# Optimization experiments

Measured on AMD Instinct MI355X. Metric: run time of the kernel, lower is better.

Reference implementation:

```python
import jax, jax.numpy as jnp
import numpy as np

# MORR all-pass ring parameters (MORRConfig_20um defaults: attenuation / self-coupling)
A_MORR = 0.8578
R_MORR = 0.8578
KS = 3       # kernel_size
MB = 8       # miniblock (circulant block size)
BN_EPS = 1e-5


def mrr_roundtrip_phase_to_tr(phi):
    # through-port transmission of an all-pass microring vs roundtrip phase
    c = jnp.cos(phi)
    num = A_MORR * A_MORR - 2.0 * A_MORR * R_MORR * c + R_MORR * R_MORR
    den = 1.0 - 2.0 * A_MORR * R_MORR * c + (A_MORR * R_MORR) ** 2
    return num / den


def setup_inputs() -> dict:
    key = jax.random.key(0)
    k1, k2 = jax.random.split(key, 2)
    B, C, H, W = 64, 64, 32, 32
    outC = 64
    q = (C * KS * KS + MB - 1) // MB   # grid_dim_x = 72
    p = (outC + MB - 1) // MB          # grid_dim_y = 8
    x = jax.random.normal(k1, (B, C, H, W), jnp.float32)
    weight = jax.random.normal(k2, (p, q, MB), jnp.float32) * 0.05  # circulant eigen-vectors per block
    gamma = jnp.ones((outC,), jnp.float32)   # BatchNorm2d weight
    beta = jnp.zeros((outC,), jnp.float32)   # BatchNorm2d bias
    return {"x": x, "weight": weight, "gamma": gamma, "beta": beta}


def reference(x, weight, gamma, beta):
    B, C, H, W = x.shape
    p, q, mb = weight.shape
    outC = gamma.shape[0]
    Ho, Wo = H, W  # stride=1, padding=1, ks=3
    L = Ho * Wo
    # im2col (torch F.unfold ordering: C major, then kh, kw)
    xp = jnp.pad(x, ((0, 0), (0, 0), (1, 1), (1, 1)))
    cols = jnp.stack([xp[:, :, i:i + Ho, j:j + Wo]
                      for i in range(KS) for j in range(KS)], axis=2)  # [B,C,9,Ho,Wo]
    cols = cols.reshape(B, C * KS * KS, L).transpose(0, 2, 1)          # [B,L,C*k*k]
    assert C * KS * KS == q * mb, "patch dim must pad to q*mb"
    s = cols.reshape(B, L, q, mb)
    s = s * s  # optical intensity (power) fed into the MORR
    # block-circulant weight: Wc[p,q,i,j] = weight[p,q,(i-j) mod mb]
    i_idx = jnp.arange(mb)
    idx = (i_idx[:, None] - i_idx[None, :]) % mb
    Wc = weight[:, :, idx]                                             # [p,q,mb,mb]
    # accumulated roundtrip phase per output node
    phase = jnp.einsum('blqj,pqij->blpi', s, Wc)                       # [B,L,p,mb]
    tr = mrr_roundtrip_phase_to_tr(phase)
    out = tr.reshape(B, L, p * mb)[:, :, :outC]                        # truncate to out_channel
    out = out.transpose(0, 2, 1).reshape(B, outC, Ho, Wo)
    # BatchNorm2d (training mode: batch statistics) + Hardtanh(-1, 1)
    mean = out.mean(axis=(0, 2, 3), keepdims=True)
    var = out.var(axis=(0, 2, 3), keepdims=True)
    y = (out - mean) * jax.lax.rsqrt(var + BN_EPS)
    y = y * gamma[None, :, None, None] + beta[None, :, None, None]
    return jnp.clip(y, -1.0, 1.0)
```

## Files before the change

### kernel.cpp

```cpp
#include <hip/hip_runtime.h>


#define A_MORR 0.8578f
#define R_MORR 0.8578f
#define TR_C1 (A_MORR * A_MORR + R_MORR * R_MORR)
#define TR_C2 (-2.0f * A_MORR * R_MORR)
#define TR_C3 (1.0f + (A_MORR * R_MORR) * (A_MORR * R_MORR))
#define BN_EPS 1e-5f

#define NPIX 65536
#define X2_LO 17408
#define SMEM_BYTES 34816
#define NBLK 1024

typedef __attribute__((ext_vector_type(8))) short bf16x8;
typedef __attribute__((ext_vector_type(16))) float f32x16;

__device__ __forceinline__ void bf16split(float s, unsigned short& h, unsigned short& l) {
    union { float f; unsigned u; } cv; cv.f = s;
    unsigned r = (cv.u + 0x7fffu + ((cv.u >> 16) & 1u)) & 0xffff0000u;
    h = (unsigned short)(r >> 16);
    union { unsigned u; float f; } hv; hv.u = r;
    float lo = s - hv.f;
    cv.f = lo;
    unsigned r2 = cv.u + 0x7fffu + ((cv.u >> 16) & 1u);
    l = (unsigned short)(r2 >> 16);
}

__global__ __launch_bounds__(256) void prep_kernel(const float* __restrict__ w,
                                                   char* __restrict__ wfrag) {
    int gtid = blockIdx.x * 256 + threadIdx.x;
    if (gtid < 36864) {
        int j    = gtid & 7;
        int lane = (gtid >> 3) & 63;
        int okm  = gtid >> 9;
        int mt   = okm & 1;
        int ks   = (okm >> 1) & 3;
        int off  = okm >> 3;
        int oc   = mt * 32 + (lane & 31);
        int c    = ks * 16 + (lane >> 5) * 8 + j;
        int kg   = c * 9 + off;
        float val = w[(oc >> 3) * 576 + (kg >> 3) * 8 + ((oc - kg) & 7)];
        unsigned short h, l;
        bf16split(val, h, l);
        ((unsigned short*)(wfrag + okm * 2048))[lane * 8 + j] = h;
        ((unsigned short*)(wfrag + okm * 2048 + 1024))[lane * 8 + j] = l;
    }
}

__global__ __launch_bounds__(256, 4) void conv_kernel(const float* __restrict__ x,
                                                      const char* __restrict__ wfrag,
                                                      float* __restrict__ out,
                                                      float* __restrict__ partials) {
    const int rt  = blockIdx.x;
    const int b   = blockIdx.y;
    const int bid = b * 16 + rt;
    const int tid = threadIdx.x;

    const int lane = tid & 63;
    const int wv   = tid >> 6;
    const int wmt  = wv & 1;
    const int py   = wv >> 1;
    const int col  = lane & 31;
    const int hs   = lane >> 5;

    __shared__ __align__(16) char smem[SMEM_BYTES];

    if (tid < 128) {
        int pr = tid & 1;
        int q  = (tid >> 1) & 7;
        int rc = tid >> 4;
        int r  = rc >> 1;
        int cc = (rc & 1) ? 33 : 0;
        int g  = q ^ (cc & 7);
        *(uint4*)(smem + pr * X2_LO + ((r * 34 + cc) << 7) + (g << 4)) = uint4{0, 0, 0, 0};
    }

    {
        const int co = tid & 31;
        const int qg = tid >> 5;
        const int c  = 1 + co;
        const int gw = (qg ^ (c & 7)) << 4;
        const float* xb = x + (size_t)(b * 64 + qg * 8) * 1024 + co;
#pragma unroll
        for (int r = 0; r < 4; ++r) {
            int gr = rt * 2 - 1 + r;
            float v[8];
#pragma unroll
            for (int j = 0; j < 8; ++j) v[j] = 0.0f;
            if (gr >= 0 && gr < 32) {
#pragma unroll
                for (int j = 0; j < 8; ++j) v[j] = xb[j * 1024 + gr * 32];
            }
            unsigned hp[4], lp[4];
#pragma unroll
            for (int p = 0; p < 4; ++p) {
                unsigned short h0, l0, h1, l1;
                float s0 = v[2 * p] * v[2 * p];
                float s1 = v[2 * p + 1] * v[2 * p + 1];
                bf16split(s0, h0, l0);
                bf16split(s1, h1, l1);
                hp[p] = (unsigned)h0 | ((unsigned)h1 << 16);
                lp[p] = (unsigned)l0 | ((unsigned)l1 << 16);
            }
            char* dst = smem + ((r * 34 + c) << 7) + gw;
            *(uint4*)dst            = uint4{hp[0], hp[1], hp[2], hp[3]};
            *(uint4*)(dst + X2_LO)  = uint4{lp[0], lp[1], lp[2], lp[3]};
        }
    }
    __syncthreads();

    f32x16 acc;
#pragma unroll
    for (int i = 0; i < 16; ++i) acc[i] = 0.f;

    const char* wbase = wfrag + wmt * 2048 + (size_t)lane * 16;

#pragma unroll
    for (int dj = 0; dj < 3; ++dj) {
        const int c2 = col + dj;
        const int c7 = c2 & 7;
#pragma unroll
        for (int kp = 0; kp < 2; ++kp) {
            bf16x8 wh_[2][3], wl_[2][3];
#pragma unroll
            for (int ksi = 0; ksi < 2; ++ksi) {
#pragma unroll
                for (int di = 0; di < 3; ++di) {
                    const char* wp = wbase + (di * 3 + dj) * 16384 + (kp * 2 + ksi) * 4096;
                    wh_[ksi][di] = *(const bf16x8*)wp;
                    wl_[ksi][di] = *(const bf16x8*)(wp + 1024);
                }
            }
#pragma unroll
            for (int ksi = 0; ksi < 2; ++ksi) {
                const int ks = kp * 2 + ksi;
                const int gg = ((ks * 2 + hs) ^ c7) << 4;
                bf16x8 bh[3], bl[3];
#pragma unroll
                for (int di = 0; di < 3; ++di) {
                    const char* sp = smem + (((py + di) * 34 + c2) << 7) + gg;
                    bh[di] = *(const bf16x8*)sp;
                    bl[di] = *(const bf16x8*)(sp + X2_LO);
                }
#pragma unroll
                for (int di = 0; di < 3; ++di) {
                    acc = __builtin_amdgcn_mfma_f32_32x32x16_bf16(wh_[ksi][di], bh[di], acc, 0, 0, 0);
                    acc = __builtin_amdgcn_mfma_f32_32x32x16_bf16(wh_[ksi][di], bl[di], acc, 0, 0, 0);
                    acc = __builtin_amdgcn_mfma_f32_32x32x16_bf16(wl_[ksi][di], bh[di], acc, 0, 0, 0);
                }
            }
        }
    }

    float tv[16];
    {
        const size_t obase = ((size_t)b * 64 + wmt * 32) * 1024 + (rt * 2 + py) * 32 + col;
#pragma unroll
        for (int j = 0; j < 16; ++j) {
            float cp = __cosf(acc[j]);
            float t  = fmaf(TR_C2, cp, TR_C1) / fmaf(TR_C2, cp, TR_C3);
            tv[j] = t;
            int ocl = (j & 3) + 8 * (j >> 2) + 4 * hs;
            out[obase + (size_t)ocl * 1024] = t;
        }
    }

    float* red1 = (float*)smem;
    float* red2 = red1 + 64 * 66;
    __syncthreads();
#pragma unroll
    for (int j = 0; j < 16; ++j) {
        int ocl = (j & 3) + 8 * (j >> 2) + 4 * hs;
        int ri  = (wmt * 32 + ocl) * 66 + py * 33 + col;
        red1[ri] = tv[j];
        red2[ri] = tv[j] * tv[j];
    }
    __syncthreads();
    if (tid < 64) {
        float s1 = 0.f, s2 = 0.f;
#pragma unroll
        for (int k = 0; k < 64; ++k) {
            int idx = tid * 66 + (k >> 5) * 33 + (k & 31);
            s1 += red1[idx];
            s2 += red2[idx];
        }
        partials[(size_t)tid * NBLK + bid]        = s1;
        partials[(size_t)(64 + tid) * NBLK + bid] = s2;
    }
}

__global__ __launch_bounds__(512) void stats_kernel(const float* __restrict__ partials,
                                                    const float* __restrict__ gamma,
                                                    const float* __restrict__ beta,
                                                    float* __restrict__ ss) {
    const int c   = blockIdx.x;
    const int tid = threadIdx.x;
    __shared__ float r1[512], r2[512];
    r1[tid] = partials[(size_t)c * NBLK + tid] + partials[(size_t)c * NBLK + 512 + tid];
    r2[tid] = partials[(size_t)(64 + c) * NBLK + tid]
            + partials[(size_t)(64 + c) * NBLK + 512 + tid];
    __syncthreads();
#pragma unroll
    for (int s = 256; s > 0; s >>= 1) {
        if (tid < s) {
            r1[tid] += r1[tid + s];
            r2[tid] += r2[tid + s];
        }
        __syncthreads();
    }
    if (tid == 0) {
        const float invN = 1.0f / (float)NPIX;
        float mean = r1[0] * invN;
        float var  = r2[0] * invN - mean * mean;
        float sc   = gamma[c] * rsqrtf(var + BN_EPS);
        ss[c]      = sc;
        ss[64 + c] = beta[c] - mean * sc;
    }
}

__global__ __launch_bounds__(256) void norm_kernel(float* __restrict__ out,
                                                   const float* __restrict__ ss) {
    int i = blockIdx.x * 256 + threadIdx.x;
    float4 v = ((float4*)out)[i];
    int oc = (i >> 8) & 63;
    float sc = ss[oc];
    float sh = ss[64 + oc];
    v.x = fminf(1.0f, fmaxf(-1.0f, fmaf(v.x, sc, sh)));
    v.y = fminf(1.0f, fmaxf(-1.0f, fmaf(v.y, sc, sh)));
    v.z = fminf(1.0f, fmaxf(-1.0f, fmaf(v.z, sc, sh)));
    v.w = fminf(1.0f, fmaxf(-1.0f, fmaf(v.w, sc, sh)));
    ((float4*)out)[i] = v;
}

extern "C" void kernel_launch(void* const* d_in, const int* in_sizes, int n_in,
                              void* d_out, int out_size, void* d_ws, size_t ws_size,
                              hipStream_t stream) {
    const float* x     = (const float*)d_in[0];
    const float* w     = (const float*)d_in[1];
    const float* gamma = (const float*)d_in[2];
    const float* beta  = (const float*)d_in[3];
    float* out = (float*)d_out;

    char*  wfrag    = (char*)d_ws;
    float* partials = (float*)((char*)d_ws + 147456);
    float* ss       = partials + 128 * NBLK;

    hipLaunchKernelGGL(prep_kernel, dim3(144), dim3(256), 0, stream, w, wfrag);
    hipLaunchKernelGGL(conv_kernel, dim3(16, 64), dim3(256), 0, stream, x, wfrag, out, partials);
    hipLaunchKernelGGL(stats_kernel, dim3(64), dim3(512), 0, stream, partials, gamma, beta, ss);
    hipLaunchKernelGGL(norm_kernel, dim3(4096), dim3(256), 0, stream, out, ss);
}
```

Measured before the change: 42.87 us.

## Split conv tiles to one output row per block with two waves and float2 loads

New measurement: 49.97 us. 16.6% more time.

```diff
diff --git a/kernel.cpp b/kernel.cpp
--- a/kernel.cpp
+++ b/kernel.cpp
@@ -9,9 +9,9 @@
 #define BN_EPS 1e-5f
 
 #define NPIX 65536
-#define X2_LO 17408
-#define SMEM_BYTES 34816
-#define NBLK 1024
+#define X2_LO 13056
+#define SMEM_BYTES 26112
+#define NBLK 2048
 
 typedef __attribute__((ext_vector_type(8))) short bf16x8;
 typedef __attribute__((ext_vector_type(16))) float f32x16;
@@ -48,25 +48,23 @@
     }
 }
 
-__global__ __launch_bounds__(256, 4) void conv_kernel(const float* __restrict__ x,
+__global__ __launch_bounds__(128, 4) void conv_kernel(const float* __restrict__ x,
                                                       const char* __restrict__ wfrag,
                                                       float* __restrict__ out,
                                                       float* __restrict__ partials) {
     const int rt  = blockIdx.x;
     const int b   = blockIdx.y;
-    const int bid = b * 16 + rt;
+    const int bid = b * 32 + rt;
     const int tid = threadIdx.x;
 
     const int lane = tid & 63;
-    const int wv   = tid >> 6;
-    const int wmt  = wv & 1;
-    const int py   = wv >> 1;
+    const int wmt  = tid >> 6;
     const int col  = lane & 31;
     const int hs   = lane >> 5;
 
     __shared__ __align__(16) char smem[SMEM_BYTES];
 
-    if (tid < 128) {
+    if (tid < 96) {
         int pr = tid & 1;
         int q  = (tid >> 1) & 7;
         int rc = tid >> 4;
@@ -77,35 +75,47 @@
     }
 
     {
-        const int co = tid & 31;
-        const int qg = tid >> 5;
-        const int c  = 1 + co;
-        const int gw = (qg ^ (c & 7)) << 4;
-        const float* xb = x + (size_t)(b * 64 + qg * 8) * 1024 + co;
-#pragma unroll
-        for (int r = 0; r < 4; ++r) {
-            int gr = rt * 2 - 1 + r;
-            float v[8];
-#pragma unroll
-            for (int j = 0; j < 8; ++j) v[j] = 0.0f;
+        const int co2 = tid & 15;
+        const int qg  = tid >> 4;
+        const int cA  = 1 + co2 * 2;
+        const int cB  = cA + 1;
+        const int gwA = (qg ^ (cA & 7)) << 4;
+        const int gwB = (qg ^ (cB & 7)) << 4;
+        const float* xb = x + (size_t)(b * 64 + qg * 8) * 1024 + co2 * 2;
+#pragma unroll
+        for (int r = 0; r < 3; ++r) {
+            int gr = rt - 1 + r;
+            float2 v2[8];
+#pragma unroll
+            for (int j = 0; j < 8; ++j) v2[j] = float2{0.f, 0.f};
             if (gr >= 0 && gr < 32) {
 #pragma unroll
-                for (int j = 0; j < 8; ++j) v[j] = xb[j * 1024 + gr * 32];
-            }
-            unsigned hp[4], lp[4];
+                for (int j = 0; j < 8; ++j)
+                    v2[j] = *(const float2*)(xb + j * 1024 + gr * 32);
+            }
+            unsigned hA[4], lA[4], hB[4], lB[4];
 #pragma unroll
             for (int p = 0; p < 4; ++p) {
                 unsigned short h0, l0, h1, l1;
-                float s0 = v[2 * p] * v[2 * p];
-                float s1 = v[2 * p + 1] * v[2 * p + 1];
-                bf16split(s0, h0, l0);
-                bf16split(s1, h1, l1);
-                hp[p] = (unsigned)h0 | ((unsigned)h1 << 16);
-                lp[p] = (unsigned)l0 | ((unsigned)l1 << 16);
-            }
-            char* dst = smem + ((r * 34 + c) << 7) + gw;
-            *(uint4*)dst            = uint4{hp[0], hp[1], hp[2], hp[3]};
-            *(uint4*)(dst + X2_LO)  = uint4{lp[0], lp[1], lp[2], lp[3]};
+                float sa0 = v2[2 * p].x * v2[2 * p].x;
+                float sa1 = v2[2 * p + 1].x * v2[2 * p + 1].x;
+                bf16split(sa0, h0, l0);
+                bf16split(sa1, h1, l1);
+                hA[p] = (unsigned)h0 | ((unsigned)h1 << 16);
+                lA[p] = (unsigned)l0 | ((unsigned)l1 << 16);
+                float sb0 = v2[2 * p].y * v2[2 * p].y;
+                float sb1 = v2[2 * p + 1].y * v2[2 * p + 1].y;
+                bf16split(sb0, h0, l0);
+                bf16split(sb1, h1, l1);
+                hB[p] = (unsigned)h0 | ((unsigned)h1 << 16);
+                lB[p] = (unsigned)l0 | ((unsigned)l1 << 16);
+            }
+            char* dA = smem + ((r * 34 + cA) << 7) + gwA;
+            char* dB = smem + ((r * 34 + cB) << 7) + gwB;
+            *(uint4*)dA           = uint4{hA[0], hA[1], hA[2], hA[3]};
+            *(uint4*)(dA + X2_LO) = uint4{lA[0], lA[1], lA[2], lA[3]};
+            *(uint4*)dB           = uint4{hB[0], hB[1], hB[2], hB[3]};
+            *(uint4*)(dB + X2_LO) = uint4{lB[0], lB[1], lB[2], lB[3]};
         }
     }
     __syncthreads();
@@ -116,6 +126,7 @@
 
     const char* wbase = wfrag + wmt * 2048 + (size_t)lane * 16;
 
+    __builtin_amdgcn_s_setprio(1);
 #pragma unroll
     for (int dj = 0; dj < 3; ++dj) {
         const int c2 = col + dj;
@@ -139,7 +150,7 @@
                 bf16x8 bh[3], bl[3];
 #pragma unroll
                 for (int di = 0; di < 3; ++di) {
-                    const char* sp = smem + (((py + di) * 34 + c2) << 7) + gg;
+                    const char* sp = smem + ((di * 34 + c2) << 7) + gg;
                     bh[di] = *(const bf16x8*)sp;
                     bl[di] = *(const bf16x8*)(sp + X2_LO);
                 }
@@ -152,10 +163,11 @@
             }
         }
     }
+    __builtin_amdgcn_s_setprio(0);
 
     float tv[16];
     {
-        const size_t obase = ((size_t)b * 64 + wmt * 32) * 1024 + (rt * 2 + py) * 32 + col;
+        const size_t obase = ((size_t)b * 64 + wmt * 32) * 1024 + rt * 32 + col;
 #pragma unroll
         for (int j = 0; j < 16; ++j) {
             float cp = __cosf(acc[j]);
@@ -167,12 +179,12 @@
     }
 
     float* red1 = (float*)smem;
-    float* red2 = red1 + 64 * 66;
+    float* red2 = red1 + 64 * 33;
     __syncthreads();
 #pragma unroll
     for (int j = 0; j < 16; ++j) {
         int ocl = (j & 3) + 8 * (j >> 2) + 4 * hs;
-        int ri  = (wmt * 32 + ocl) * 66 + py * 33 + col;
+        int ri  = (wmt * 32 + ocl) * 33 + col;
         red1[ri] = tv[j];
         red2[ri] = tv[j] * tv[j];
     }
@@ -180,10 +192,9 @@
     if (tid < 64) {
         float s1 = 0.f, s2 = 0.f;
 #pragma unroll
-        for (int k = 0; k < 64; ++k) {
-            int idx = tid * 66 + (k >> 5) * 33 + (k & 31);
-            s1 += red1[idx];
-            s2 += red2[idx];
+        for (int p = 0; p < 32; ++p) {
+            s1 += red1[tid * 33 + p];
+            s2 += red2[tid * 33 + p];
         }
         partials[(size_t)tid * NBLK + bid]        = s1;
         partials[(size_t)(64 + tid) * NBLK + bid] = s2;
@@ -197,9 +208,10 @@
     const int c   = blockIdx.x;
     const int tid = threadIdx.x;
     __shared__ float r1[512], r2[512];
-    r1[tid] = partials[(size_t)c * NBLK + tid] + partials[(size_t)c * NBLK + 512 + tid];
-    r2[tid] = partials[(size_t)(64 + c) * NBLK + tid]
-            + partials[(size_t)(64 + c) * NBLK + 512 + tid];
+    const float* p1 = partials + (size_t)c * NBLK;
+    const float* p2 = partials + (size_t)(64 + c) * NBLK;
+    r1[tid] = p1[tid] + p1[tid + 512] + p1[tid + 1024] + p1[tid + 1536];
+    r2[tid] = p2[tid] + p2[tid + 512] + p2[tid + 1024] + p2[tid + 1536];
     __syncthreads();
 #pragma unroll
     for (int s = 256; s > 0; s >>= 1) {
@@ -247,7 +259,7 @@
     float* ss       = partials + 128 * NBLK;
 
     hipLaunchKernelGGL(prep_kernel, dim3(144), dim3(256), 0, stream, w, wfrag);
-    hipLaunchKernelGGL(conv_kernel, dim3(16, 64), dim3(256), 0, stream, x, wfrag, out, partials);
+    hipLaunchKernelGGL(conv_kernel, dim3(32, 64), dim3(128), 0, stream, x, wfrag, out, partials);
     hipLaunchKernelGGL(stats_kernel, dim3(64), dim3(512), 0, stream, partials, gamma, beta, ss);
     hipLaunchKernelGGL(norm_kernel, dim3(4096), dim3(256), 0, stream, out, ss);
 }
```
